# Performance work log

Hardware: AMD Instinct MI355X
Metric: run time of the kernel (lower is better)

The kernel has to match this reference:

```python
import jax, jax.numpy as jnp
import numpy as np

M, B, T, D, P = 3, 128, 512, 1024, 256  # modalities, batch, time, d_model, projection_dim
LN_EPS = 1e-5
NORM_EPS = 1e-12


def setup_inputs() -> dict:
    key = jax.random.key(0)
    ks = jax.random.split(key, 7)
    s1 = 1.0 / np.sqrt(D)
    s2 = 1.0 / np.sqrt(D)
    return {
        "feats": jax.random.normal(ks[0], (M, B, T, D), dtype=jnp.float32),
        "W1": jax.random.uniform(ks[1], (M, D, D), jnp.float32, -s1, s1),
        "b1": jax.random.uniform(ks[2], (M, D), jnp.float32, -s1, s1),
        "W2": jax.random.uniform(ks[3], (M, D, P), jnp.float32, -s2, s2),
        "b2": jax.random.uniform(ks[4], (M, P), jnp.float32, -s2, s2),
        "gamma": jnp.ones((M, P), jnp.float32),
        "beta": jnp.zeros((M, P), jnp.float32),
    }


def reference(feats, W1, b1, W2, b2, gamma, beta):
    # Mean-pool over time: [M,B,T,D] -> [M,B,D]
    pooled = feats.mean(axis=2)
    # Linear(d_model, d_model) + exact GELU (dropout is identity at inference)
    h = jax.nn.gelu(jnp.einsum('mbd,mde->mbe', pooled, W1) + b1[:, None, :],
                    approximate=False)
    # Linear(d_model, projection_dim)
    z = jnp.einsum('mbd,mdp->mbp', h, W2) + b2[:, None, :]
    # LayerNorm over last dim
    mu = z.mean(axis=-1, keepdims=True)
    var = jnp.mean((z - mu) ** 2, axis=-1, keepdims=True)
    z = (z - mu) / jnp.sqrt(var + LN_EPS) * gamma[:, None, :] + beta[:, None, :]
    # F.normalize (cosine path): divide by max(l2_norm, eps)
    n = jnp.sqrt(jnp.sum(z * z, axis=-1, keepdims=True))
    return z / jnp.maximum(n, NORM_EPS)  # [M, B, P]
```

## Files before the change

### kernel.cpp

```cpp
#include <hip/hip_runtime.h>
#include <math.h>

#define M_ 3
#define B_ 128
#define T_ 512
#define D_ 1024
#define P_ 256
#define TC 2

#define NPOOL   (M_ * B_ * TC)
#define NW1T    192
#define NW2     64

typedef __attribute__((ext_vector_type(8))) short short8v;
typedef __attribute__((ext_vector_type(4))) float f32x4;

__device__ __forceinline__ unsigned int f2bf(float f) {
    unsigned int x = __float_as_uint(f);
    return (x + 0x7fffu + ((x >> 16) & 1u)) >> 16;
}

__global__ __launch_bounds__(256) void pool_and_cast(const float* __restrict__ feats,
                                                     const float* __restrict__ W1,
                                                     const float* __restrict__ W2,
                                                     float* __restrict__ partial,
                                                     short* __restrict__ w1t,
                                                     unsigned int* __restrict__ w2p) {
    __shared__ float ldsf[64][68];
    int blk = blockIdx.x;
    int tid = threadIdx.x;

    if (blk < NPOOL) {
        int tc = blk & (TC - 1);
        int mb = blk / TC;
        const int TSTEP = T_ / TC;
        const float4* src = (const float4*)feats + ((size_t)mb * T_ + (size_t)tc * TSTEP) * (D_ / 4) + tid;
        float4 a0 = make_float4(0.f, 0.f, 0.f, 0.f);
        float4 a1 = a0, a2 = a0, a3 = a0, a4 = a0, a5 = a0, a6 = a0, a7 = a0;
        for (int t = 0; t < TSTEP; t += 8) {
            float4 v0 = src[0 * (D_ / 4)];
            float4 v1 = src[1 * (D_ / 4)];
            float4 v2 = src[2 * (D_ / 4)];
            float4 v3 = src[3 * (D_ / 4)];
            float4 v4 = src[4 * (D_ / 4)];
            float4 v5 = src[5 * (D_ / 4)];
            float4 v6 = src[6 * (D_ / 4)];
            float4 v7 = src[7 * (D_ / 4)];
            src += 8 * (D_ / 4);
            a0.x += v0.x; a0.y += v0.y; a0.z += v0.z; a0.w += v0.w;
            a1.x += v1.x; a1.y += v1.y; a1.z += v1.z; a1.w += v1.w;
            a2.x += v2.x; a2.y += v2.y; a2.z += v2.z; a2.w += v2.w;
            a3.x += v3.x; a3.y += v3.y; a3.z += v3.z; a3.w += v3.w;
            a4.x += v4.x; a4.y += v4.y; a4.z += v4.z; a4.w += v4.w;
            a5.x += v5.x; a5.y += v5.y; a5.z += v5.z; a5.w += v5.w;
            a6.x += v6.x; a6.y += v6.y; a6.z += v6.z; a6.w += v6.w;
            a7.x += v7.x; a7.y += v7.y; a7.z += v7.z; a7.w += v7.w;
        }
        float4 s;
        s.x = ((a0.x + a1.x) + (a2.x + a3.x)) + ((a4.x + a5.x) + (a6.x + a7.x));
        s.y = ((a0.y + a1.y) + (a2.y + a3.y)) + ((a4.y + a5.y) + (a6.y + a7.y));
        s.z = ((a0.z + a1.z) + (a2.z + a3.z)) + ((a4.z + a5.z) + (a6.z + a7.z));
        s.w = ((a0.w + a1.w) + (a2.w + a3.w)) + ((a4.w + a5.w) + (a6.w + a7.w));
        ((float4*)partial)[((size_t)mb * TC + tc) * (D_ / 4) + tid] = s;
        return;
    }

    if (blk < NPOOL + NW1T) {
        int bid = blk - NPOOL;
        for (int i = 0; i < 4; ++i) {
            int tile = bid * 4 + i;
            int et = tile & 15;
            int kt = (tile >> 4) & 15;
            int mm = tile >> 8;
            int k0 = kt * 64, ee0 = et * 64;
#pragma unroll
            for (int sv = 0; sv < 4; ++sv) {
                int idx = sv * 256 + tid;
                int row = idx >> 4;
                int c4  = idx & 15;
                float4 v = *(const float4*)(W1 + (size_t)mm * D_ * D_ + (size_t)(k0 + row) * D_ + ee0 + c4 * 4);
                *(float4*)&ldsf[row][c4 * 4] = v;
            }
            __syncthreads();
            int er = tid >> 2;
            int ks = (tid & 3) * 16;
            short8v v0, v1;
#pragma unroll
            for (int j = 0; j < 8; ++j) v0[j] = (short)f2bf(ldsf[ks + j][er]);
#pragma unroll
            for (int j = 0; j < 8; ++j) v1[j] = (short)f2bf(ldsf[ks + 8 + j][er]);
            size_t ob = ((size_t)mm * D_ + ee0 + er) * D_ + k0 + ks;
            *(short8v*)(w1t + ob)     = v0;
            *(short8v*)(w1t + ob + 8) = v1;
            __syncthreads();
        }
        return;
    }

    {
        int bid = blk - NPOOL - NW1T;
        const int TOT = M_ * (D_ / 2) * P_;
        for (int i = bid * 256 + tid; i < TOT; i += NW2 * 256) {
            int p  = i & (P_ - 1);
            int k2 = (i >> 8) & (D_ / 2 - 1);
            int m  = i >> 17;
            size_t base = (size_t)m * D_ * P_ + (size_t)(2 * k2) * P_ + p;
            float f0 = W2[base];
            float f1 = W2[base + P_];
            w2p[i] = f2bf(f0) | (f2bf(f1) << 16);
        }
    }
}

__global__ __launch_bounds__(256) void gemm1_mfma(const float* __restrict__ partial,
                                                  const short* __restrict__ w1t,
                                                  const float* __restrict__ b1,
                                                  float* __restrict__ h) {
    __shared__ __align__(16) short As[32 * 64];
    __shared__ __align__(16) short Bs[64 * 64];
    int m  = blockIdx.z;
    int b0 = blockIdx.y * 32;
    int e0 = blockIdx.x * 64;
    int tid = threadIdx.x;
    int l   = tid & 63;
    int w   = tid >> 6;
    int wr  = w & 1, wc = w >> 1;

    int arow = tid >> 3;
    int k8   = tid & 7;
    int bcol = tid >> 2;
    int bj   = tid & 3;

    const float* Abase = partial + ((size_t)(m * B_ + b0 + arow) * TC) * D_ + k8 * 8;
    const short* Bbase = w1t + ((size_t)m * D_ + e0 + bcol) * D_ + bj * 16;

    char* AsB = (char*)As;
    char* BsB = (char*)Bs;
    short8v* AsW  = (short8v*)(AsB + arow * 128 + ((k8 ^ (arow & 7)) << 4));
    short8v* BsW0 = (short8v*)(BsB + bcol * 128 + (((2 * bj)     ^ (bcol & 7)) << 4));
    short8v* BsW1 = (short8v*)(BsB + bcol * 128 + (((2 * bj + 1) ^ (bcol & 7)) << 4));

    f32x4 acc0 = {0.f, 0.f, 0.f, 0.f};
    f32x4 acc1 = {0.f, 0.f, 0.f, 0.f};
    const float inv = 1.0f / (float)T_;

    int ar  = wr * 16 + (l & 15);
    int bc0 = wc * 32 + (l & 15);
    int bc1 = bc0 + 16;
    int lh  = l >> 4;

    for (int it = 0; it < 16; ++it) {
        int k0 = it * 64;
        float4 p00 = *(const float4*)(Abase + k0);
        float4 p01 = *(const float4*)(Abase + k0 + 4);
        float4 p10 = *(const float4*)(Abase + D_ + k0);
        float4 p11 = *(const float4*)(Abase + D_ + k0 + 4);
        short8v bv0 = *(const short8v*)(Bbase + k0);
        short8v bv1 = *(const short8v*)(Bbase + k0 + 8);
        __syncthreads();
        short8v av;
        av[0] = (short)f2bf((p00.x + p10.x) * inv);
        av[1] = (short)f2bf((p00.y + p10.y) * inv);
        av[2] = (short)f2bf((p00.z + p10.z) * inv);
        av[3] = (short)f2bf((p00.w + p10.w) * inv);
        av[4] = (short)f2bf((p01.x + p11.x) * inv);
        av[5] = (short)f2bf((p01.y + p11.y) * inv);
        av[6] = (short)f2bf((p01.z + p11.z) * inv);
        av[7] = (short)f2bf((p01.w + p11.w) * inv);
        *AsW  = av;
        *BsW0 = bv0;
        *BsW1 = bv1;
        __syncthreads();
#pragma unroll
        for (int kk = 0; kk < 2; ++kk) {
            int ch = kk * 4 + lh;
            short8v af  = *(const short8v*)(AsB + ar  * 128 + ((ch ^ (ar  & 7)) << 4));
            short8v bf0 = *(const short8v*)(BsB + bc0 * 128 + ((ch ^ (bc0 & 7)) << 4));
            short8v bf1 = *(const short8v*)(BsB + bc1 * 128 + ((ch ^ (bc1 & 7)) << 4));
            acc0 = __builtin_amdgcn_mfma_f32_16x16x32_bf16(af, bf0, acc0, 0, 0, 0);
            acc1 = __builtin_amdgcn_mfma_f32_16x16x32_bf16(af, bf1, acc1, 0, 0, 0);
        }
    }

    int colBase = e0 + wc * 32 + (l & 15);
    int rowBase = b0 + wr * 16 + lh * 4;
    const float is2 = 0.70710678118654752f;
#pragma unroll
    for (int n = 0; n < 2; ++n) {
        f32x4 acc = n ? acc1 : acc0;
        int col = colBase + n * 16;
        float bb = b1[m * D_ + col];
#pragma unroll
        for (int r = 0; r < 4; ++r) {
            float x = acc[r] + bb;
            float gx = 0.5f * x * (1.0f + erff(x * is2));
            h[(size_t)(m * B_ + rowBase + r) * D_ + col] = gx;
        }
    }
}

__global__ __launch_bounds__(512) void gemm2_ln(const float* __restrict__ h,
                                                const unsigned int* __restrict__ w2p,
                                                const float* __restrict__ b2,
                                                const float* __restrict__ gamma,
                                                const float* __restrict__ beta,
                                                float* __restrict__ out) {
    int m  = blockIdx.y;
    int b0 = blockIdx.x * 2;
    int tid  = threadIdx.x;
    int p    = tid & 255;
    int half = tid >> 8;
    int lane = tid & 63;
    int w    = (tid >> 6) & 3;

    __shared__ float accs[2][2][256];
    __shared__ float redA[2][4];
    __shared__ float redB[2][4];
    __shared__ float redC[2][4];

    const unsigned int* Wp = w2p + (size_t)m * (D_ / 2) * P_ + (size_t)half * 256 * P_ + p;
    const float* hb = h + ((size_t)m * B_ + b0) * D_ + half * 512;

    float acc0 = 0.f, acc1 = 0.f;
#pragma unroll 4
    for (int q = 0; q < 128; ++q) {
        unsigned int u0 = Wp[(size_t)(2 * q) * P_];
        unsigned int u1 = Wp[(size_t)(2 * q + 1) * P_];
        float w0 = __uint_as_float(u0 << 16);
        float w1 = __uint_as_float(u0 & 0xffff0000u);
        float w2 = __uint_as_float(u1 << 16);
        float w3 = __uint_as_float(u1 & 0xffff0000u);
        float4 h0 = *(const float4*)(hb + 4 * q);
        float4 h1 = *(const float4*)(hb + D_ + 4 * q);
        acc0 += h0.x * w0 + h0.y * w1 + h0.z * w2 + h0.w * w3;
        acc1 += h1.x * w0 + h1.y * w1 + h1.z * w2 + h1.w * w3;
    }
    accs[half][0][p] = acc0;
    accs[half][1][p] = acc1;
    __syncthreads();

    int g = half;
    float z = accs[0][g][p] + accs[1][g][p] + b2[m * P_ + p];

    float s1 = z, s2 = z * z;
    for (int off = 32; off > 0; off >>= 1) {
        s1 += __shfl_xor(s1, off);
        s2 += __shfl_xor(s2, off);
    }
    if (lane == 0) { redA[g][w] = s1; redB[g][w] = s2; }
    __syncthreads();
    s1 = (redA[g][0] + redA[g][1]) + (redA[g][2] + redA[g][3]);
    s2 = (redB[g][0] + redB[g][1]) + (redB[g][2] + redB[g][3]);
    float mu  = s1 * (1.0f / P_);
    float var = s2 * (1.0f / P_) - mu * mu;
    float inv = 1.0f / sqrtf(var + 1e-5f);
    z = (z - mu) * inv * gamma[m * P_ + p] + beta[m * P_ + p];

    float s = z * z;
    for (int off = 32; off > 0; off >>= 1) s += __shfl_xor(s, off);
    if (lane == 0) redC[g][w] = s;
    __syncthreads();
    s = (redC[g][0] + redC[g][1]) + (redC[g][2] + redC[g][3]);
    float n = sqrtf(s);
    out[((size_t)m * B_ + b0 + g) * P_ + p] = z / fmaxf(n, 1e-12f);
}

extern "C" void kernel_launch(void* const* d_in, const int* in_sizes, int n_in,
                              void* d_out, int out_size, void* d_ws, size_t ws_size,
                              hipStream_t stream) {
    const float* feats = (const float*)d_in[0];
    const float* W1    = (const float*)d_in[1];
    const float* b1    = (const float*)d_in[2];
    const float* W2    = (const float*)d_in[3];
    const float* b2    = (const float*)d_in[4];
    const float* gamma = (const float*)d_in[5];
    const float* beta  = (const float*)d_in[6];
    float* out = (float*)d_out;

    float* wsf = (float*)d_ws;
    float*        partial = wsf;
    unsigned int* w2p     = (unsigned int*)(wsf + 786432);
    float*        hbuf    = wsf + 786432 + 393216;
    short*        w1t     = (short*)(wsf + 786432 + 2 * 393216);

    pool_and_cast<<<NPOOL + NW1T + NW2, 256, 0, stream>>>(feats, W1, W2, partial, w1t, w2p);
    dim3 g2(D_ / 64, B_ / 32, M_);
    gemm1_mfma<<<g2, 256, 0, stream>>>(partial, w1t, b1, hbuf);
    dim3 g3(B_ / 2, M_);
    gemm2_ln<<<g3, 512, 0, stream>>>(hbuf, w2p, b2, gamma, beta, out);
}
```

Baseline: 193.5 us.

## Fuse three kernels into one cooperative kernel with grid-wide syncs

```diff
diff --git a/kernel.cpp b/kernel.cpp
--- a/kernel.cpp
+++ b/kernel.cpp
@@ -1,5 +1,8 @@
 #include <hip/hip_runtime.h>
+#include <hip/hip_cooperative_groups.h>
 #include <math.h>
+
+namespace cg = cooperative_groups;
 
 #define M_ 3
 #define B_ 128
@@ -11,6 +14,7 @@
 #define NPOOL   (M_ * B_ * TC)
 #define NW1T    192
 #define NW2     64
+#define NBLK    (NPOOL + NW1T + NW2)
 
 typedef __attribute__((ext_vector_type(8))) short short8v;
 typedef __attribute__((ext_vector_type(4))) float f32x4;
@@ -20,108 +24,98 @@
     return (x + 0x7fffu + ((x >> 16) & 1u)) >> 16;
 }
 
-__global__ __launch_bounds__(256) void pool_and_cast(const float* __restrict__ feats,
-                                                     const float* __restrict__ W1,
-                                                     const float* __restrict__ W2,
-                                                     float* __restrict__ partial,
-                                                     short* __restrict__ w1t,
-                                                     unsigned int* __restrict__ w2p) {
-    __shared__ float ldsf[64][68];
-    int blk = blockIdx.x;
-    int tid = threadIdx.x;
-
-    if (blk < NPOOL) {
-        int tc = blk & (TC - 1);
-        int mb = blk / TC;
-        const int TSTEP = T_ / TC;
-        const float4* src = (const float4*)feats + ((size_t)mb * T_ + (size_t)tc * TSTEP) * (D_ / 4) + tid;
-        float4 a0 = make_float4(0.f, 0.f, 0.f, 0.f);
-        float4 a1 = a0, a2 = a0, a3 = a0, a4 = a0, a5 = a0, a6 = a0, a7 = a0;
-        for (int t = 0; t < TSTEP; t += 8) {
-            float4 v0 = src[0 * (D_ / 4)];
-            float4 v1 = src[1 * (D_ / 4)];
-            float4 v2 = src[2 * (D_ / 4)];
-            float4 v3 = src[3 * (D_ / 4)];
-            float4 v4 = src[4 * (D_ / 4)];
-            float4 v5 = src[5 * (D_ / 4)];
-            float4 v6 = src[6 * (D_ / 4)];
-            float4 v7 = src[7 * (D_ / 4)];
-            src += 8 * (D_ / 4);
-            a0.x += v0.x; a0.y += v0.y; a0.z += v0.z; a0.w += v0.w;
-            a1.x += v1.x; a1.y += v1.y; a1.z += v1.z; a1.w += v1.w;
-            a2.x += v2.x; a2.y += v2.y; a2.z += v2.z; a2.w += v2.w;
-            a3.x += v3.x; a3.y += v3.y; a3.z += v3.z; a3.w += v3.w;
-            a4.x += v4.x; a4.y += v4.y; a4.z += v4.z; a4.w += v4.w;
-            a5.x += v5.x; a5.y += v5.y; a5.z += v5.z; a5.w += v5.w;
-            a6.x += v6.x; a6.y += v6.y; a6.z += v6.z; a6.w += v6.w;
-            a7.x += v7.x; a7.y += v7.y; a7.z += v7.z; a7.w += v7.w;
+__device__ __forceinline__ void pool_block(const float* __restrict__ feats,
+                                           float* __restrict__ partial,
+                                           int blk, int tid) {
+    int tc = blk & (TC - 1);
+    int mb = blk / TC;
+    const int TSTEP = T_ / TC;
+    const int LDQ = D_ / 4;
+    const float4* src = (const float4*)feats + ((size_t)mb * T_ + (size_t)tc * TSTEP) * LDQ + tid;
+    float4 a0 = make_float4(0.f, 0.f, 0.f, 0.f);
+    float4 a1 = a0, a2 = a0, a3 = a0, a4 = a0, a5 = a0, a6 = a0, a7 = a0;
+    for (int t = 0; t < TSTEP; t += 8) {
+        float4 v0 = src[0 * LDQ];
+        float4 v1 = src[1 * LDQ];
+        float4 v2 = src[2 * LDQ];
+        float4 v3 = src[3 * LDQ];
+        float4 v4 = src[4 * LDQ];
+        float4 v5 = src[5 * LDQ];
+        float4 v6 = src[6 * LDQ];
+        float4 v7 = src[7 * LDQ];
+        src += 8 * LDQ;
+        a0.x += v0.x; a0.y += v0.y; a0.z += v0.z; a0.w += v0.w;
+        a1.x += v1.x; a1.y += v1.y; a1.z += v1.z; a1.w += v1.w;
+        a2.x += v2.x; a2.y += v2.y; a2.z += v2.z; a2.w += v2.w;
+        a3.x += v3.x; a3.y += v3.y; a3.z += v3.z; a3.w += v3.w;
+        a4.x += v4.x; a4.y += v4.y; a4.z += v4.z; a4.w += v4.w;
+        a5.x += v5.x; a5.y += v5.y; a5.z += v5.z; a5.w += v5.w;
+        a6.x += v6.x; a6.y += v6.y; a6.z += v6.z; a6.w += v6.w;
+        a7.x += v7.x; a7.y += v7.y; a7.z += v7.z; a7.w += v7.w;
+    }
+    float4 s;
+    s.x = ((a0.x + a1.x) + (a2.x + a3.x)) + ((a4.x + a5.x) + (a6.x + a7.x));
+    s.y = ((a0.y + a1.y) + (a2.y + a3.y)) + ((a4.y + a5.y) + (a6.y + a7.y));
+    s.z = ((a0.z + a1.z) + (a2.z + a3.z)) + ((a4.z + a5.z) + (a6.z + a7.z));
+    s.w = ((a0.w + a1.w) + (a2.w + a3.w)) + ((a4.w + a5.w) + (a6.w + a7.w));
+    ((float4*)partial)[((size_t)mb * TC + tc) * (D_ / 4) + tid] = s;
+}
+
+__device__ __forceinline__ void w1t_block(const float* __restrict__ W1,
+                                          short* __restrict__ w1t,
+                                          int bid, int tid, float (*ldsf)[68]) {
+    for (int i = 0; i < 4; ++i) {
+        int tile = bid * 4 + i;
+        int et = tile & 15;
+        int kt = (tile >> 4) & 15;
+        int mm = tile >> 8;
+        int k0 = kt * 64, ee0 = et * 64;
+#pragma unroll
+        for (int sv = 0; sv < 4; ++sv) {
+            int idx = sv * 256 + tid;
+            int row = idx >> 4;
+            int c4  = idx & 15;
+            float4 v = *(const float4*)(W1 + (size_t)mm * D_ * D_ + (size_t)(k0 + row) * D_ + ee0 + c4 * 4);
+            *(float4*)&ldsf[row][c4 * 4] = v;
         }
-        float4 s;
-        s.x = ((a0.x + a1.x) + (a2.x + a3.x)) + ((a4.x + a5.x) + (a6.x + a7.x));
-        s.y = ((a0.y + a1.y) + (a2.y + a3.y)) + ((a4.y + a5.y) + (a6.y + a7.y));
-        s.z = ((a0.z + a1.z) + (a2.z + a3.z)) + ((a4.z + a5.z) + (a6.z + a7.z));
-        s.w = ((a0.w + a1.w) + (a2.w + a3.w)) + ((a4.w + a5.w) + (a6.w + a7.w));
-        ((float4*)partial)[((size_t)mb * TC + tc) * (D_ / 4) + tid] = s;
-        return;
-    }
-
-    if (blk < NPOOL + NW1T) {
-        int bid = blk - NPOOL;
-        for (int i = 0; i < 4; ++i) {
-            int tile = bid * 4 + i;
-            int et = tile & 15;
-            int kt = (tile >> 4) & 15;
-            int mm = tile >> 8;
-            int k0 = kt * 64, ee0 = et * 64;
-#pragma unroll
-            for (int sv = 0; sv < 4; ++sv) {
-                int idx = sv * 256 + tid;
-                int row = idx >> 4;
-                int c4  = idx & 15;
-                float4 v = *(const float4*)(W1 + (size_t)mm * D_ * D_ + (size_t)(k0 + row) * D_ + ee0 + c4 * 4);
-                *(float4*)&ldsf[row][c4 * 4] = v;
-            }
-            __syncthreads();
-            int er = tid >> 2;
-            int ks = (tid & 3) * 16;
-            short8v v0, v1;
-#pragma unroll
-            for (int j = 0; j < 8; ++j) v0[j] = (short)f2bf(ldsf[ks + j][er]);
-#pragma unroll
-            for (int j = 0; j < 8; ++j) v1[j] = (short)f2bf(ldsf[ks + 8 + j][er]);
-            size_t ob = ((size_t)mm * D_ + ee0 + er) * D_ + k0 + ks;
-            *(short8v*)(w1t + ob)     = v0;
-            *(short8v*)(w1t + ob + 8) = v1;
-            __syncthreads();
-        }
-        return;
-    }
-
-    {
-        int bid = blk - NPOOL - NW1T;
-        const int TOT = M_ * (D_ / 2) * P_;
-        for (int i = bid * 256 + tid; i < TOT; i += NW2 * 256) {
-            int p  = i & (P_ - 1);
-            int k2 = (i >> 8) & (D_ / 2 - 1);
-            int m  = i >> 17;
-            size_t base = (size_t)m * D_ * P_ + (size_t)(2 * k2) * P_ + p;
-            float f0 = W2[base];
-            float f1 = W2[base + P_];
-            w2p[i] = f2bf(f0) | (f2bf(f1) << 16);
-        }
-    }
-}
-
-__global__ __launch_bounds__(256) void gemm1_mfma(const float* __restrict__ partial,
-                                                  const short* __restrict__ w1t,
-                                                  const float* __restrict__ b1,
-                                                  float* __restrict__ h) {
-    __shared__ __align__(16) short As[32 * 64];
-    __shared__ __align__(16) short Bs[64 * 64];
-    int m  = blockIdx.z;
-    int b0 = blockIdx.y * 32;
-    int e0 = blockIdx.x * 64;
-    int tid = threadIdx.x;
+        __syncthreads();
+        int er = tid >> 2;
+        int ks = (tid & 3) * 16;
+        short8v v0, v1;
+#pragma unroll
+        for (int j = 0; j < 8; ++j) v0[j] = (short)f2bf(ldsf[ks + j][er]);
+#pragma unroll
+        for (int j = 0; j < 8; ++j) v1[j] = (short)f2bf(ldsf[ks + 8 + j][er]);
+        size_t ob = ((size_t)mm * D_ + ee0 + er) * D_ + k0 + ks;
+        *(short8v*)(w1t + ob)     = v0;
+        *(short8v*)(w1t + ob + 8) = v1;
+        __syncthreads();
+    }
+}
+
+__device__ __forceinline__ void w2c_block(const float* __restrict__ W2,
+                                          unsigned int* __restrict__ w2p,
+                                          int bid, int tid) {
+    const int TOT = M_ * (D_ / 2) * P_;
+    for (int i = bid * 256 + tid; i < TOT; i += NW2 * 256) {
+        int p  = i & (P_ - 1);
+        int k2 = (i >> 8) & (D_ / 2 - 1);
+        int m  = i >> 17;
+        size_t base = (size_t)m * D_ * P_ + (size_t)(2 * k2) * P_ + p;
+        float f0 = W2[base];
+        float f1 = W2[base + P_];
+        w2p[i] = f2bf(f0) | (f2bf(f1) << 16);
+    }
+}
+
+__device__ __forceinline__ void gemm1_block(const float* __restrict__ partial,
+                                            const short* __restrict__ w1t,
+                                            const float* __restrict__ b1,
+                                            float* __restrict__ h,
+                                            int m, int by, int bx, int tid,
+                                            char* AsB, char* BsB) {
+    int b0 = by * 32;
+    int e0 = bx * 64;
     int l   = tid & 63;
     int w   = tid >> 6;
     int wr  = w & 1, wc = w >> 1;
@@ -134,8 +128,6 @@
     const float* Abase = partial + ((size_t)(m * B_ + b0 + arow) * TC) * D_ + k8 * 8;
     const short* Bbase = w1t + ((size_t)m * D_ + e0 + bcol) * D_ + bj * 16;
 
-    char* AsB = (char*)As;
-    char* BsB = (char*)Bs;
     short8v* AsW  = (short8v*)(AsB + arow * 128 + ((k8 ^ (arow & 7)) << 4));
     short8v* BsW0 = (short8v*)(BsB + bcol * 128 + (((2 * bj)     ^ (bcol & 7)) << 4));
     short8v* BsW1 = (short8v*)(BsB + bcol * 128 + (((2 * bj + 1) ^ (bcol & 7)) << 4));
@@ -199,70 +191,124 @@
     }
 }
 
-__global__ __launch_bounds__(512) void gemm2_ln(const float* __restrict__ h,
-                                                const unsigned int* __restrict__ w2p,
-                                                const float* __restrict__ b2,
-                                                const float* __restrict__ gamma,
-                                                const float* __restrict__ beta,
-                                                float* __restrict__ out) {
-    int m  = blockIdx.y;
-    int b0 = blockIdx.x * 2;
-    int tid  = threadIdx.x;
-    int p    = tid & 255;
-    int half = tid >> 8;
-    int lane = tid & 63;
-    int w    = (tid >> 6) & 3;
-
-    __shared__ float accs[2][2][256];
-    __shared__ float redA[2][4];
-    __shared__ float redB[2][4];
-    __shared__ float redC[2][4];
-
-    const unsigned int* Wp = w2p + (size_t)m * (D_ / 2) * P_ + (size_t)half * 256 * P_ + p;
-    const float* hb = h + ((size_t)m * B_ + b0) * D_ + half * 512;
-
+__device__ __forceinline__ void gemm2_block(const float* __restrict__ h,
+                                            const unsigned int* __restrict__ w2p,
+                                            const float* __restrict__ b2,
+                                            const float* __restrict__ gamma,
+                                            const float* __restrict__ beta,
+                                            float* __restrict__ out,
+                                            int m, int b0, int tid,
+                                            float* hs0, float* hs1, float* red) {
+    const float* hrow = h + (size_t)(m * B_ + b0) * D_;
+    ((float4*)hs0)[tid] = ((const float4*)hrow)[tid];
+    ((float4*)hs1)[tid] = ((const float4*)(hrow + D_))[tid];
+    __syncthreads();
+    const unsigned int* Wp = w2p + (size_t)m * (D_ / 2) * P_ + tid;
     float acc0 = 0.f, acc1 = 0.f;
-#pragma unroll 4
-    for (int q = 0; q < 128; ++q) {
-        unsigned int u0 = Wp[(size_t)(2 * q) * P_];
-        unsigned int u1 = Wp[(size_t)(2 * q + 1) * P_];
-        float w0 = __uint_as_float(u0 << 16);
-        float w1 = __uint_as_float(u0 & 0xffff0000u);
-        float w2 = __uint_as_float(u1 << 16);
-        float w3 = __uint_as_float(u1 & 0xffff0000u);
-        float4 h0 = *(const float4*)(hb + 4 * q);
-        float4 h1 = *(const float4*)(hb + D_ + 4 * q);
-        acc0 += h0.x * w0 + h0.y * w1 + h0.z * w2 + h0.w * w3;
-        acc1 += h1.x * w0 + h1.y * w1 + h1.z * w2 + h1.w * w3;
-    }
-    accs[half][0][p] = acc0;
-    accs[half][1][p] = acc1;
+#pragma unroll 8
+    for (int k2 = 0; k2 < D_ / 2; ++k2) {
+        unsigned int u = Wp[(size_t)k2 * P_];
+        float w0 = __uint_as_float(u << 16);
+        float w1 = __uint_as_float(u & 0xffff0000u);
+        float h00 = hs0[2 * k2], h01 = hs0[2 * k2 + 1];
+        float h10 = hs1[2 * k2], h11 = hs1[2 * k2 + 1];
+        acc0 += h00 * w0 + h01 * w1;
+        acc1 += h10 * w0 + h11 * w1;
+    }
+    int lane = tid & 63, w = tid >> 6;
+    float bias = b2[m * P_ + tid], gm = gamma[m * P_ + tid], bt = beta[m * P_ + tid];
+    float z0 = acc0 + bias, z1 = acc1 + bias;
+
+    float s10 = z0, s20 = z0 * z0, s11 = z1, s21 = z1 * z1;
+    for (int off = 32; off; off >>= 1) {
+        s10 += __shfl_xor(s10, off); s20 += __shfl_xor(s20, off);
+        s11 += __shfl_xor(s11, off); s21 += __shfl_xor(s21, off);
+    }
+    if (lane == 0) { red[w] = s10; red[4 + w] = s20; red[8 + w] = s11; red[12 + w] = s21; }
     __syncthreads();
-
-    int g = half;
-    float z = accs[0][g][p] + accs[1][g][p] + b2[m * P_ + p];
-
-    float s1 = z, s2 = z * z;
-    for (int off = 32; off > 0; off >>= 1) {
-        s1 += __shfl_xor(s1, off);
-        s2 += __shfl_xor(s2, off);
-    }
-    if (lane == 0) { redA[g][w] = s1; redB[g][w] = s2; }
+    {
+        float s1 = (red[0] + red[1]) + (red[2] + red[3]);
+        float s2 = (red[4] + red[5]) + (red[6] + red[7]);
+        float mu = s1 * (1.0f / P_), var = s2 * (1.0f / P_) - mu * mu;
+        float iv = 1.0f / sqrtf(var + 1e-5f);
+        z0 = (z0 - mu) * iv * gm + bt;
+        float s1b = (red[8] + red[9]) + (red[10] + red[11]);
+        float s2b = (red[12] + red[13]) + (red[14] + red[15]);
+        float mub = s1b * (1.0f / P_), varb = s2b * (1.0f / P_) - mub * mub;
+        float ivb = 1.0f / sqrtf(varb + 1e-5f);
+        z1 = (z1 - mub) * ivb * gm + bt;
+    }
     __syncthreads();
-    s1 = (redA[g][0] + redA[g][1]) + (redA[g][2] + redA[g][3]);
-    s2 = (redB[g][0] + redB[g][1]) + (redB[g][2] + redB[g][3]);
-    float mu  = s1 * (1.0f / P_);
-    float var = s2 * (1.0f / P_) - mu * mu;
-    float inv = 1.0f / sqrtf(var + 1e-5f);
-    z = (z - mu) * inv * gamma[m * P_ + p] + beta[m * P_ + p];
-
-    float s = z * z;
-    for (int off = 32; off > 0; off >>= 1) s += __shfl_xor(s, off);
-    if (lane == 0) redC[g][w] = s;
+    float t0 = z0 * z0, t1 = z1 * z1;
+    for (int off = 32; off; off >>= 1) { t0 += __shfl_xor(t0, off); t1 += __shfl_xor(t1, off); }
+    if (lane == 0) { red[w] = t0; red[4 + w] = t1; }
     __syncthreads();
-    s = (redC[g][0] + redC[g][1]) + (redC[g][2] + redC[g][3]);
-    float n = sqrtf(s);
-    out[((size_t)m * B_ + b0 + g) * P_ + p] = z / fmaxf(n, 1e-12f);
+    float n0 = sqrtf((red[0] + red[1]) + (red[2] + red[3]));
+    float n1 = sqrtf((red[4] + red[5]) + (red[6] + red[7]));
+    out[(size_t)(m * B_ + b0) * P_ + tid]     = z0 / fmaxf(n0, 1e-12f);
+    out[(size_t)(m * B_ + b0 + 1) * P_ + tid] = z1 / fmaxf(n1, 1e-12f);
+}
+
+__global__ __launch_bounds__(256, 4) void fused_all(const float* feats, const float* W1,
+                                                    const float* W2, const float* b1,
+                                                    const float* b2, const float* gamma,
+                                                    const float* beta, float* partial,
+                                                    short* w1t, unsigned int* w2p,
+                                                    float* hbuf, float* out) {
+    __shared__ __align__(16) char smem[17408];
+    int blk = blockIdx.x;
+    int tid = threadIdx.x;
+
+    if (blk < NPOOL) {
+        pool_block(feats, partial, blk, tid);
+    } else if (blk < NPOOL + NW1T) {
+        w1t_block(W1, w1t, blk - NPOOL, tid, (float(*)[68])smem);
+    } else {
+        w2c_block(W2, w2p, blk - NPOOL - NW1T, tid);
+    }
+    cg::this_grid().sync();
+
+    if (blk < 192) {
+        int m = blk >> 6, rem = blk & 63;
+        gemm1_block(partial, w1t, b1, hbuf, m, rem >> 4, rem & 15, tid,
+                    smem, smem + 4096);
+    }
+    cg::this_grid().sync();
+
+    if (blk < 192) {
+        int m = blk >> 6, b0 = (blk & 63) * 2;
+        gemm2_block(hbuf, w2p, b2, gamma, beta, out, m, b0, tid,
+                    (float*)smem, (float*)(smem + 4096), (float*)(smem + 8192));
+    }
+}
+
+__global__ __launch_bounds__(256) void pool_cast_k(const float* feats, const float* W1,
+                                                   const float* W2, float* partial,
+                                                   short* w1t, unsigned int* w2p) {
+    __shared__ __align__(16) char smem[17408];
+    int blk = blockIdx.x, tid = threadIdx.x;
+    if (blk < NPOOL) pool_block(feats, partial, blk, tid);
+    else if (blk < NPOOL + NW1T) w1t_block(W1, w1t, blk - NPOOL, tid, (float(*)[68])smem);
+    else w2c_block(W2, w2p, blk - NPOOL - NW1T, tid);
+}
+
+__global__ __launch_bounds__(256) void gemm1_k(const float* partial, const short* w1t,
+                                               const float* b1, float* hbuf) {
+    __shared__ __align__(16) char smem[12288];
+    int blk = blockIdx.x;
+    int m = blk >> 6, rem = blk & 63;
+    gemm1_block(partial, w1t, b1, hbuf, m, rem >> 4, rem & 15, threadIdx.x,
+                smem, smem + 4096);
+}
+
+__global__ __launch_bounds__(256) void gemm2_k(const float* hbuf, const unsigned int* w2p,
+                                               const float* b2, const float* gamma,
+                                               const float* beta, float* out) {
+    __shared__ __align__(16) char smem[8320];
+    int blk = blockIdx.x;
+    int m = blk >> 6, b0 = (blk & 63) * 2;
+    gemm2_block(hbuf, w2p, b2, gamma, beta, out, m, b0, threadIdx.x,
+                (float*)smem, (float*)(smem + 4096), (float*)(smem + 8192));
 }
 
 extern "C" void kernel_launch(void* const* d_in, const int* in_sizes, int n_in,
@@ -283,9 +329,14 @@
     float*        hbuf    = wsf + 786432 + 393216;
     short*        w1t     = (short*)(wsf + 786432 + 2 * 393216);
 
-    pool_and_cast<<<NPOOL + NW1T + NW2, 256, 0, stream>>>(feats, W1, W2, partial, w1t, w2p);
-    dim3 g2(D_ / 64, B_ / 32, M_);
-    gemm1_mfma<<<g2, 256, 0, stream>>>(partial, w1t, b1, hbuf);
-    dim3 g3(B_ / 2, M_);
-    gemm2_ln<<<g3, 512, 0, stream>>>(hbuf, w2p, b2, gamma, beta, out);
-}
+    void* kargs[] = {(void*)&feats, (void*)&W1, (void*)&W2, (void*)&b1, (void*)&b2,
+                     (void*)&gamma, (void*)&beta, (void*)&partial, (void*)&w1t,
+                     (void*)&w2p, (void*)&hbuf, (void*)&out};
+    hipError_t e = hipLaunchCooperativeKernel((void*)fused_all, dim3(NBLK), dim3(256),
+                                              kargs, 0, stream);
+    if (e != hipSuccess) {
+        pool_cast_k<<<NBLK, 256, 0, stream>>>(feats, W1, W2, partial, w1t, w2p);
+        gemm1_k<<<192, 256, 0, stream>>>(partial, w1t, b1, hbuf);
+        gemm2_k<<<192, 256, 0, stream>>>(hbuf, w2p, b2, gamma, beta, out);
+    }
+}
```

New measurement: 443.6 us. 2.29x slower.
